# Kernel tuning notes

Measured on AMD Instinct MI355X. Metric: run time of the kernel, lower is better.

The kernel has to match this reference:

```python
import jax, jax.numpy as jnp
import numpy as np

B, LQ, LK, E, H = 8, 1024, 1024, 512, 8
D = E // H
NEG = -2.0**32 + 1  # padding value used by original torch code


def setup_inputs() -> dict:
    key = jax.random.key(0)
    ks = jax.random.split(key, 6)
    s = 0.02
    return {
        "x1": jax.random.normal(ks[0], (B, LQ, E), jnp.float32),
        "x2": jax.random.normal(ks[1], (B, LK, E), jnp.float32),
        "Wq": jax.random.normal(ks[2], (E, E), jnp.float32) * s,
        "bq": jnp.zeros((E,), jnp.float32),
        "Wk": jax.random.normal(ks[3], (E, E), jnp.float32) * s,
        "bk": jnp.zeros((E,), jnp.float32),
        "Wv": jax.random.normal(ks[4], (E, E), jnp.float32) * s,
        "bv": jnp.zeros((E,), jnp.float32),
    }


def _split_heads(t):
    # torch: cat(split(t, E//H, dim=2), dim=0) -> head-major [H, B, L, D]
    b, l, _ = t.shape
    return jnp.moveaxis(t.reshape(b, l, H, D), 2, 0)


def reference(x1, x2, Wq, bq, Wk, bk, Wv, bv):
    # ReLU-activated projections (nn.Linear: x @ W.T + b)
    q = jax.nn.relu(x1 @ Wq.T + bq)  # [B,LQ,E]
    k = jax.nn.relu(x2 @ Wk.T + bk)  # [B,LK,E]
    v = jax.nn.relu(x2 @ Wv.T + bv)  # [B,LK,E]

    q_, k_, v_ = _split_heads(q), _split_heads(k), _split_heads(v)  # [H,B,L,D]

    # scaled scores; original scales by sqrt(emb_size), not sqrt(d_head)
    scores = jnp.einsum('hbqd,hbkd->hbqk', q_, k_) / jnp.sqrt(jnp.float32(E))

    # sin-based key mask from raw x2
    key_mask = jnp.sin(jnp.abs(jnp.sum(x2, -1)))  # [B,LK]
    scores = jnp.where(key_mask[None, :, None, :] <= 0, NEG, scores)

    attn = jax.nn.softmax(scores, axis=-1)

    # sin-based query mask from raw x1, applied after softmax
    query_mask = jnp.sin(jnp.abs(jnp.sum(x1, -1)))  # [B,LQ]
    attn = attn * query_mask[None, :, :, None]

    out = jnp.einsum('hbqk,hbkd->hbqd', attn, v_)  # [H,B,LQ,D]
    out = jnp.moveaxis(out, 0, 2).reshape(B, LQ, E)  # merge heads back
    return out + q  # residual add with activated query projection
```

## Files before the change

### kernel.cpp

```cpp
#include <hip/hip_runtime.h>
#include <hip/hip_bf16.h>
#include <math.h>

typedef short bf16x8 __attribute__((ext_vector_type(8)));
typedef float f32x4 __attribute__((ext_vector_type(4)));
typedef unsigned int u32;
typedef unsigned short u16;

constexpr int Bb = 8, LQn = 1024, LKn = 1024, En = 512, Hn = 8, Dn = 64;
constexpr int Mtok = Bb * LQn;
constexpr float KCOEF = 0.06376246332977306f;

__device__ __forceinline__ u16 f2bf(float f) {
  u32 u = __builtin_bit_cast(u32, f);
  u32 r = (u + 0x7fffu + ((u >> 16) & 1u)) >> 16;
  return (u16)r;
}
__device__ __forceinline__ float bf2f(u16 h) {
  u32 u = ((u32)h) << 16;
  return __builtin_bit_cast(float, u);
}
__device__ __forceinline__ u16 f2bf_hw(float f) {
  return __builtin_bit_cast(u16, __float2bfloat16(f));
}

__device__ __forceinline__ void async_lds16(const void* gsrc, void* ldst) {
  __builtin_amdgcn_global_load_lds(
      (const __attribute__((address_space(1))) u32*)gsrc,
      (__attribute__((address_space(3))) u32*)ldst, 16, 0, 0);
}

__global__ void cvtmask2_kernel(const float* __restrict__ x1, const float* __restrict__ x2,
                                u16* __restrict__ x1b, u16* __restrict__ x2b,
                                float* __restrict__ qmask, float* __restrict__ kmask) {
  int id = blockIdx.x * 4 + (threadIdx.x >> 6);
  int lane = threadIdx.x & 63;
  const float* x; u16* xb; float* mask; int row;
  if (id < Mtok) { x = x1; xb = x1b; mask = qmask; row = id; }
  else           { x = x2; xb = x2b; mask = kmask; row = id - Mtok; }
  const float4* p = reinterpret_cast<const float4*>(x + (size_t)row * En);
  ushort4* ob = reinterpret_cast<ushort4*>(xb + (size_t)row * En);
  double s = 0.0;
#pragma unroll
  for (int j = 0; j < En / 256; ++j) {
    float4 v = p[lane + j * 64];
    s += (double)v.x + (double)v.y + (double)v.z + (double)v.w;
    ushort4 o;
    o.x = f2bf(v.x); o.y = f2bf(v.y); o.z = f2bf(v.z); o.w = f2bf(v.w);
    ob[lane + j * 64] = o;
  }
#pragma unroll
  for (int off = 32; off > 0; off >>= 1) s += __shfl_down(s, off, 64);
  if (lane == 0) mask[row] = (float)sin(fabs(s));
}

__global__ void cvt3_kernel(const float* __restrict__ a, const float* __restrict__ b,
                            const float* __restrict__ c, u16* __restrict__ oa,
                            u16* __restrict__ ob, u16* __restrict__ oc, int n4) {
  int i = blockIdx.x * blockDim.x + threadIdx.x;
  const float* src;
  u16* dst;
  int j = i;
  if (j < n4) { src = a; dst = oa; }
  else if (j < 2 * n4) { src = b; dst = ob; j -= n4; }
  else { src = c; dst = oc; j -= 2 * n4; }
  float4 v = reinterpret_cast<const float4*>(src)[j];
  ushort4 o;
  o.x = f2bf(v.x); o.y = f2bf(v.y); o.z = f2bf(v.z); o.w = f2bf(v.w);
  reinterpret_cast<ushort4*>(dst)[j] = o;
}

template <int BIAS_ROW, int XROW>
__global__ __launch_bounds__(256, 2) void gemm_bt_relu(
    const u16* __restrict__ A, const u16* __restrict__ Bm,
    const float* __restrict__ bias, u16* __restrict__ C,
    int ldc, float coef) {
  constexpr int K = 512, BM = 128, BN = 64, BK = 64;
  __shared__ u16 sA[2][BM * BK];
  __shared__ u16 sB[2][BN * BK];
  int tid = threadIdx.x;
  int lane = tid & 63;
  int w = tid >> 6;
  int row0 = (XROW ? blockIdx.x : blockIdx.y) * BM;
  int col0 = (XROW ? blockIdx.y : blockIdx.x) * BN;
  int wm = w >> 1, wn = w & 1;
  int rgrp = lane >> 4, cidx = lane & 15;

  f32x4 acc[4][2];
#pragma unroll
  for (int mi = 0; mi < 4; ++mi)
#pragma unroll
    for (int ni = 0; ni < 2; ++ni) acc[mi][ni] = f32x4{0.f, 0.f, 0.f, 0.f};

  auto stage = [&](int kt, int buf) {
    int k0 = kt * BK;
#pragma unroll
    for (int rr = 0; rr < 4; ++rr) {
      int cid = rr * 256 + tid;
      int r = cid >> 3, c = cid & 7;
      int cg = c ^ (r & 7);
      async_lds16(A + (size_t)(row0 + r) * K + k0 + cg * 8, &sA[buf][cid * 8]);
    }
#pragma unroll
    for (int rr = 0; rr < 2; ++rr) {
      int cid = rr * 256 + tid;
      int r = cid >> 3, c = cid & 7;
      int cg = c ^ (r & 7);
      async_lds16(Bm + (size_t)(col0 + r) * K + k0 + cg * 8, &sB[buf][cid * 8]);
    }
  };

  stage(0, 0);
  __syncthreads();

  for (int kt = 0; kt < K / BK; ++kt) {
    int cur = kt & 1;
    if (kt < K / BK - 1) stage(kt + 1, cur ^ 1);
#pragma unroll
    for (int kk = 0; kk < 2; ++kk) {
      bf16x8 a[4], b[2];
#pragma unroll
      for (int mi = 0; mi < 4; ++mi) {
        int row = wm * 64 + mi * 16 + cidx;
        a[mi] = *reinterpret_cast<const bf16x8*>(
            &sA[cur][row * BK + ((kk * 4 + rgrp) ^ (row & 7)) * 8]);
      }
#pragma unroll
      for (int ni = 0; ni < 2; ++ni) {
        int row = wn * 32 + ni * 16 + cidx;
        b[ni] = *reinterpret_cast<const bf16x8*>(
            &sB[cur][row * BK + ((kk * 4 + rgrp) ^ (row & 7)) * 8]);
      }
#pragma unroll
      for (int mi = 0; mi < 4; ++mi)
#pragma unroll
        for (int ni = 0; ni < 2; ++ni)
          acc[mi][ni] = __builtin_amdgcn_mfma_f32_16x16x32_bf16(a[mi], b[ni], acc[mi][ni], 0, 0, 0);
    }
    __syncthreads();
  }
#pragma unroll
  for (int mi = 0; mi < 4; ++mi)
#pragma unroll
    for (int ni = 0; ni < 2; ++ni)
#pragma unroll
      for (int r = 0; r < 4; ++r) {
        int grow = row0 + wm * 64 + mi * 16 + rgrp * 4 + r;
        int gcol = col0 + wn * 32 + ni * 16 + cidx;
        float v = acc[mi][ni][r] + (BIAS_ROW ? bias[grow] : bias[gcol]);
        v = v > 0.f ? v : 0.f;
        C[(size_t)grow * ldc + gcol] = f2bf(v * coef);
      }
}

__global__ __launch_bounds__(256, 4) void attn_kernel(
    const u16* __restrict__ qb, const u16* __restrict__ kb, const u16* __restrict__ vtb,
    const float* __restrict__ kmask, const float* __restrict__ qmask,
    float* __restrict__ out) {
  __shared__ u16 sK[2][64 * 64];
  __shared__ u16 sV[2][64 * 64];
  __shared__ u16 sQP[64 * 64];
  int tid = threadIdx.x, lane = tid & 63, w = tid >> 6;
  int bh = blockIdx.x, qblk = blockIdx.y;
  int b = bh >> 3, h = bh & 7;
  int rgrp = lane >> 4, cidx = lane & 15;

  const u16* qbase = qb + ((size_t)(b * LQn) + qblk * 64) * En + h * Dn;
  const u16* kbase = kb + (size_t)(b * LKn) * En + h * Dn;
  const u16* vbase = vtb + (size_t)(h * Dn) * Mtok + b * LKn;
  const float* kmb = kmask + b * LKn;

  auto stageKV = [&](int kt, int buf) {
#pragma unroll
    for (int rr = 0; rr < 2; ++rr) {
      int cid = rr * 256 + tid;
      int r = cid >> 3, c = cid & 7;
      int cg = c ^ (r & 7);
      async_lds16(kbase + (size_t)(kt * 64 + r) * En + cg * 8, &sK[buf][cid * 8]);
      async_lds16(vbase + (size_t)r * Mtok + kt * 64 + cg * 8, &sV[buf][cid * 8]);
    }
  };

#pragma unroll
  for (int rr = 0; rr < 2; ++rr) {
    int cid = rr * 256 + tid;
    int r = cid >> 3, c = cid & 7;
    int cg = c ^ (r & 7);
    async_lds16(qbase + (size_t)r * En + cg * 8, &sQP[cid * 8]);
  }
  stageKV(0, 0);
  __syncthreads();

  bf16x8 qa[2];
  {
    int row = w * 16 + cidx;
    qa[0] = *reinterpret_cast<const bf16x8*>(&sQP[row * 64 + (rgrp ^ (row & 7)) * 8]);
    qa[1] = *reinterpret_cast<const bf16x8*>(&sQP[row * 64 + ((4 + rgrp) ^ (row & 7)) * 8]);
  }

  f32x4 acc_o[4];
#pragma unroll
  for (int dt = 0; dt < 4; ++dt) acc_o[dt] = f32x4{0.f, 0.f, 0.f, 0.f};
  float den[4] = {0.f, 0.f, 0.f, 0.f};

  for (int kt = 0; kt < LKn / 64; ++kt) {
    int cur = kt & 1;
    if (kt < LKn / 64 - 1) stageKV(kt + 1, cur ^ 1);
#pragma unroll
    for (int ktile = 0; ktile < 4; ++ktile) {
      int krow = ktile * 16 + cidx;
      bf16x8 kf0 = *reinterpret_cast<const bf16x8*>(
          &sK[cur][krow * 64 + (rgrp ^ (krow & 7)) * 8]);
      bf16x8 kf1 = *reinterpret_cast<const bf16x8*>(
          &sK[cur][krow * 64 + ((4 + rgrp) ^ (krow & 7)) * 8]);
      f32x4 s = f32x4{0.f, 0.f, 0.f, 0.f};
      s = __builtin_amdgcn_mfma_f32_16x16x32_bf16(qa[0], kf0, s, 0, 0, 0);
      s = __builtin_amdgcn_mfma_f32_16x16x32_bf16(qa[1], kf1, s, 0, 0, 0);
      float km = kmb[kt * 64 + ktile * 16 + cidx];
      bool on = km > 0.f;
#pragma unroll
      for (int r = 0; r < 4; ++r) {
        float p = on ? __builtin_amdgcn_exp2f(s[r]) : 0.f;
        den[r] += p;
        int prow = w * 16 + rgrp * 4 + r;
        sQP[prow * 64 + ((ktile * 16 + cidx) ^ ((prow & 7) << 3))] = f2bf_hw(p);
      }
    }
#pragma unroll
    for (int kk = 0; kk < 2; ++kk) {
      int prow = w * 16 + cidx;
      bf16x8 pa = *reinterpret_cast<const bf16x8*>(
          &sQP[prow * 64 + ((kk * 4 + rgrp) ^ (prow & 7)) * 8]);
#pragma unroll
      for (int dt = 0; dt < 4; ++dt) {
        int vrow = dt * 16 + cidx;
        bf16x8 vf = *reinterpret_cast<const bf16x8*>(
            &sV[cur][vrow * 64 + ((kk * 4 + rgrp) ^ (vrow & 7)) * 8]);
        acc_o[dt] = __builtin_amdgcn_mfma_f32_16x16x32_bf16(pa, vf, acc_o[dt], 0, 0, 0);
      }
    }
    __syncthreads();
  }
#pragma unroll
  for (int r = 0; r < 4; ++r)
#pragma unroll
    for (int off = 8; off > 0; off >>= 1) den[r] += __shfl_xor(den[r], off, 64);

  const float* qmb = qmask + (size_t)b * LQn + qblk * 64 + w * 16;
  const u16* qres = qbase + (size_t)(w * 16) * En;
  float* obase = out + ((size_t)(b * LQn) + qblk * 64 + w * 16) * En + h * Dn;
#pragma unroll
  for (int r = 0; r < 4; ++r) {
    int qr = rgrp * 4 + r;
    float fac = qmb[qr] / den[r];
#pragma unroll
    for (int dt = 0; dt < 4; ++dt) {
      float v = acc_o[dt][r] * fac + bf2f(qres[(size_t)qr * En + dt * 16 + cidx]);
      obase[(size_t)qr * En + dt * 16 + cidx] = v;
    }
  }
}

extern "C" void kernel_launch(void* const* d_in, const int* in_sizes, int n_in,
                              void* d_out, int out_size, void* d_ws, size_t ws_size,
                              hipStream_t stream) {
  const float* x1 = (const float*)d_in[0];
  const float* x2 = (const float*)d_in[1];
  const float* Wq = (const float*)d_in[2];
  const float* bq = (const float*)d_in[3];
  const float* Wk = (const float*)d_in[4];
  const float* bk = (const float*)d_in[5];
  const float* Wv = (const float*)d_in[6];
  const float* bv = (const float*)d_in[7];
  float* out = (float*)d_out;

  char* ws = (char*)d_ws;
  size_t o = 0;
  u16* x1b = (u16*)(ws + o); o += (size_t)Mtok * En * 2;
  u16* x2b = (u16*)(ws + o); o += (size_t)Mtok * En * 2;
  u16* wqb = (u16*)(ws + o); o += (size_t)En * En * 2;
  u16* wkb = (u16*)(ws + o); o += (size_t)En * En * 2;
  u16* wvb = (u16*)(ws + o); o += (size_t)En * En * 2;
  u16* qbq = (u16*)(ws + o); o += (size_t)Mtok * En * 2;
  u16* kbk = (u16*)(ws + o); o += (size_t)Mtok * En * 2;
  u16* vtb = (u16*)(ws + o); o += (size_t)Mtok * En * 2;
  float* kmask = (float*)(ws + o); o += (size_t)Mtok * 4;
  float* qmask = (float*)(ws + o); o += (size_t)Mtok * 4;

  cvtmask2_kernel<<<2 * Mtok / 4, 256, 0, stream>>>(x1, x2, x1b, x2b, qmask, kmask);

  int n4w = En * En / 4;
  cvt3_kernel<<<3 * n4w / 256, 256, 0, stream>>>(Wq, Wk, Wv, wqb, wkb, wvb, n4w);

  dim3 gq(Mtok / 128, En / 64);
  gemm_bt_relu<0, 1><<<gq, 256, 0, stream>>>(x1b, wqb, bq, qbq, En, 1.0f);
  gemm_bt_relu<0, 1><<<gq, 256, 0, stream>>>(x2b, wkb, bk, kbk, En, KCOEF);
  dim3 gv(Mtok / 64, En / 128);
  gemm_bt_relu<1, 0><<<gv, 256, 0, stream>>>(wvb, x2b, bv, vtb, Mtok, 1.0f);

  dim3 ga(Bb * Hn, LQn / 64);
  attn_kernel<<<ga, 256, 0, stream>>>(qbq, kbk, vtb, kmask, qmask, out);
}
```

Baseline: 78.46 us.

## Enlarge GEMM and attention tiles to 512 threads and merge Q/K projection launches

GEMM tiles grow to 128x128 with 8 waves, and the Q and K projections are merged into one launch via blockIdx.z, which cuts launch count and reuses each staged tile across more output. The attention kernel handles 128 query rows per block with 8 waves, so each K/V tile staged in shared memory serves twice as many queries. The key mask is folded into the MFMA accumulator init as a large negative value, which removes the per-element select. Larger blocks may lower occupancy and raise register pressure, and the GEMM interior for the new wave layout is not fully shown.

```diff
diff --git a/kernel.cpp b/kernel.cpp
--- a/kernel.cpp
+++ b/kernel.cpp
@@ -70,20 +70,18 @@
   reinterpret_cast<ushort4*>(dst)[j] = o;
 }
 
-template <int BIAS_ROW, int XROW>
-__global__ __launch_bounds__(256, 2) void gemm_bt_relu(
+template <int BIAS_ROW>
+__device__ __forceinline__ void gemm_core(
     const u16* __restrict__ A, const u16* __restrict__ Bm,
     const float* __restrict__ bias, u16* __restrict__ C,
-    int ldc, float coef) {
-  constexpr int K = 512, BM = 128, BN = 64, BK = 64;
-  __shared__ u16 sA[2][BM * BK];
-  __shared__ u16 sB[2][BN * BK];
+    int ldc, float coef, int row0, int col0) {
+  constexpr int K = 512, BK = 64;
+  __shared__ u16 sA[2][128 * BK];
+  __shared__ u16 sB[2][128 * BK];
   int tid = threadIdx.x;
   int lane = tid & 63;
   int w = tid >> 6;
-  int row0 = (XROW ? blockIdx.x : blockIdx.y) * BM;
-  int col0 = (XROW ? blockIdx.y : blockIdx.x) * BN;
-  int wm = w >> 1, wn = w & 1;
+  int wm = w >> 2, wn = w & 3;
   int rgrp = lane >> 4, cidx = lane & 15;
 
   f32x4 acc[4][2];
@@ -95,15 +93,15 @@
   auto stage = [&](int kt, int buf) {
     int k0 = kt * BK;
 #pragma unroll
-    for (int rr = 0; rr < 4; ++rr) {
-      int cid = rr * 256 + tid;
+    for (int rr = 0; rr < 2; ++rr) {
+      int cid = rr * 512 + tid;
       int r = cid >> 3, c = cid & 7;
       int cg = c ^ (r & 7);
       async_lds16(A + (size_t)(row0 + r) * K + k0 + cg * 8, &sA[buf][cid * 8]);
     }
 #pragma unroll
     for (int rr = 0; rr < 2; ++rr) {
-      int cid = rr * 256 + tid;
+      int cid = rr * 512 + tid;
       int r = cid >> 3, c = cid & 7;
       int cg = c ^ (r & 7);
       async_lds16(Bm + (size_t)(col0 + r) * K + k0 + cg * 8, &sB[buf][cid * 8]);
@@ -153,37 +151,53 @@
       }
 }
 
-__global__ __launch_bounds__(256, 4) void attn_kernel(
+__global__ __launch_bounds__(512, 4) void gemm_qk(
+    const u16* __restrict__ x1b, const u16* __restrict__ wqb, const float* __restrict__ bq,
+    u16* __restrict__ qbq,
+    const u16* __restrict__ x2b, const u16* __restrict__ wkb, const float* __restrict__ bk,
+    u16* __restrict__ kbk) {
+  int z = blockIdx.z;
+  const u16* A = z ? x2b : x1b;
+  const u16* Bm = z ? wkb : wqb;
+  const float* bias = z ? bk : bq;
+  u16* C = z ? kbk : qbq;
+  float coef = z ? KCOEF : 1.0f;
+  gemm_core<0>(A, Bm, bias, C, En, coef, blockIdx.x * 128, blockIdx.y * 128);
+}
+
+__global__ __launch_bounds__(512, 4) void gemm_v(
+    const u16* __restrict__ wvb, const u16* __restrict__ x2b,
+    const float* __restrict__ bv, u16* __restrict__ vtb) {
+  gemm_core<1>(wvb, x2b, bv, vtb, Mtok, 1.0f, blockIdx.y * 128, blockIdx.x * 128);
+}
+
+__global__ __launch_bounds__(512, 6) void attn_kernel(
     const u16* __restrict__ qb, const u16* __restrict__ kb, const u16* __restrict__ vtb,
     const float* __restrict__ kmask, const float* __restrict__ qmask,
     float* __restrict__ out) {
   __shared__ u16 sK[2][64 * 64];
   __shared__ u16 sV[2][64 * 64];
-  __shared__ u16 sQP[64 * 64];
+  __shared__ u16 sQP[128 * 64];
   int tid = threadIdx.x, lane = tid & 63, w = tid >> 6;
   int bh = blockIdx.x, qblk = blockIdx.y;
   int b = bh >> 3, h = bh & 7;
   int rgrp = lane >> 4, cidx = lane & 15;
 
-  const u16* qbase = qb + ((size_t)(b * LQn) + qblk * 64) * En + h * Dn;
+  const u16* qbase = qb + ((size_t)(b * LQn) + qblk * 128) * En + h * Dn;
   const u16* kbase = kb + (size_t)(b * LKn) * En + h * Dn;
   const u16* vbase = vtb + (size_t)(h * Dn) * Mtok + b * LKn;
   const float* kmb = kmask + b * LKn;
 
   auto stageKV = [&](int kt, int buf) {
-#pragma unroll
-    for (int rr = 0; rr < 2; ++rr) {
-      int cid = rr * 256 + tid;
-      int r = cid >> 3, c = cid & 7;
-      int cg = c ^ (r & 7);
-      async_lds16(kbase + (size_t)(kt * 64 + r) * En + cg * 8, &sK[buf][cid * 8]);
-      async_lds16(vbase + (size_t)r * Mtok + kt * 64 + cg * 8, &sV[buf][cid * 8]);
-    }
+    int r = tid >> 3, c = tid & 7;
+    int cg = c ^ (r & 7);
+    async_lds16(kbase + (size_t)(kt * 64 + r) * En + cg * 8, &sK[buf][tid * 8]);
+    async_lds16(vbase + (size_t)r * Mtok + kt * 64 + cg * 8, &sV[buf][tid * 8]);
   };
 
 #pragma unroll
   for (int rr = 0; rr < 2; ++rr) {
-    int cid = rr * 256 + tid;
+    int cid = rr * 512 + tid;
     int r = cid >> 3, c = cid & 7;
     int cg = c ^ (r & 7);
     async_lds16(qbase + (size_t)r * En + cg * 8, &sQP[cid * 8]);
@@ -213,14 +227,13 @@
           &sK[cur][krow * 64 + (rgrp ^ (krow & 7)) * 8]);
       bf16x8 kf1 = *reinterpret_cast<const bf16x8*>(
           &sK[cur][krow * 64 + ((4 + rgrp) ^ (krow & 7)) * 8]);
-      f32x4 s = f32x4{0.f, 0.f, 0.f, 0.f};
+      float sinit = (kmb[kt * 64 + ktile * 16 + cidx] > 0.f) ? 0.f : -3.0e38f;
+      f32x4 s = f32x4{sinit, sinit, sinit, sinit};
       s = __builtin_amdgcn_mfma_f32_16x16x32_bf16(qa[0], kf0, s, 0, 0, 0);
       s = __builtin_amdgcn_mfma_f32_16x16x32_bf16(qa[1], kf1, s, 0, 0, 0);
-      float km = kmb[kt * 64 + ktile * 16 + cidx];
-      bool on = km > 0.f;
 #pragma unroll
       for (int r = 0; r < 4; ++r) {
-        float p = on ? __builtin_amdgcn_exp2f(s[r]) : 0.f;
+        float p = __builtin_amdgcn_exp2f(s[r]);
         den[r] += p;
         int prow = w * 16 + rgrp * 4 + r;
         sQP[prow * 64 + ((ktile * 16 + cidx) ^ ((prow & 7) << 3))] = f2bf_hw(p);
@@ -246,9 +259,9 @@
 #pragma unroll
     for (int off = 8; off > 0; off >>= 1) den[r] += __shfl_xor(den[r], off, 64);
 
-  const float* qmb = qmask + (size_t)b * LQn + qblk * 64 + w * 16;
+  const float* qmb = qmask + (size_t)b * LQn + qblk * 128 + w * 16;
   const u16* qres = qbase + (size_t)(w * 16) * En;
-  float* obase = out + ((size_t)(b * LQn) + qblk * 64 + w * 16) * En + h * Dn;
+  float* obase = out + ((size_t)(b * LQn) + qblk * 128 + w * 16) * En + h * Dn;
 #pragma unroll
   for (int r = 0; r < 4; ++r) {
     int qr = rgrp * 4 + r;
@@ -292,12 +305,11 @@
   int n4w = En * En / 4;
   cvt3_kernel<<<3 * n4w / 256, 256, 0, stream>>>(Wq, Wk, Wv, wqb, wkb, wvb, n4w);
 
-  dim3 gq(Mtok / 128, En / 64);
-  gemm_bt_relu<0, 1><<<gq, 256, 0, stream>>>(x1b, wqb, bq, qbq, En, 1.0f);
-  gemm_bt_relu<0, 1><<<gq, 256, 0, stream>>>(x2b, wkb, bk, kbk, En, KCOEF);
-  dim3 gv(Mtok / 64, En / 128);
-  gemm_bt_relu<1, 0><<<gv, 256, 0, stream>>>(wvb, x2b, bv, vtb, Mtok, 1.0f);
-
-  dim3 ga(Bb * Hn, LQn / 64);
-  attn_kernel<<<ga, 256, 0, stream>>>(qbq, kbk, vtb, kmask, qmask, out);
-}
+  dim3 gqk(Mtok / 128, En / 128, 2);
+  gemm_qk<<<gqk, 512, 0, stream>>>(x1b, wqb, bq, qbq, x2b, wkb, bk, kbk);
+  dim3 gv(Mtok / 128, En / 128);
+  gemm_v<<<gv, 512, 0, stream>>>(wvb, x2b, bv, vtb);
+
+  dim3 ga(Bb * Hn, LQn / 128);
+  attn_kernel<<<ga, 512, 0, stream>>>(qbq, kbk, vtb, kmask, qmask, out);
+}
```

After: 90.41 us. 1.15x slower.
